# Kernel tuning notes

Hardware: AMD Instinct MI355X
Metric: run time of the kernel (lower is better)

Reference implementation:

```python
import jax, jax.numpy as jnp
import numpy as np

B, T, S, D, F = 4, 2048, 2048, 256, 1024
EPS = 1e-5


def setup_inputs() -> dict:
    key = jax.random.key(0)
    ks = jax.random.split(key, 24)
    def lin(kw, kb, din, dout):
        w = jax.random.normal(kw, (din, dout), jnp.float32) / np.sqrt(din)
        b = jax.random.normal(kb, (dout,), jnp.float32) * 0.01
        return w, b
    Wq1, bq1 = lin(ks[0], ks[1], D, D)
    Wk1, bk1 = lin(ks[2], ks[3], D, D)
    Wv1, bv1 = lin(ks[4], ks[5], D, D)
    Wq2, bq2 = lin(ks[6], ks[7], D, D)
    Wk2, bk2 = lin(ks[8], ks[9], D, D)
    Wv2, bv2 = lin(ks[10], ks[11], D, D)
    W1, b1 = lin(ks[12], ks[13], D, F)
    W2, b2 = lin(ks[14], ks[15], F, D)
    y = jax.random.normal(ks[16], (B, T, D), jnp.float32)
    Z = jax.random.normal(ks[17], (B, S, D), jnp.float32)
    target_mask = jnp.tril(jnp.ones((T, T), jnp.int32))  # causal 0/1 mask
    return dict(y=y, Z=Z, target_mask=target_mask,
                Wq1=Wq1, bq1=bq1, Wk1=Wk1, bk1=bk1, Wv1=Wv1, bv1=bv1,
                Wq2=Wq2, bq2=bq2, Wk2=Wk2, bk2=bk2, Wv2=Wv2, bv2=bv2,
                W1=W1, b1=b1, W2=W2, b2=b2,
                g1=jnp.ones((D,), jnp.float32), be1=jnp.zeros((D,), jnp.float32),
                g2=jnp.ones((D,), jnp.float32), be2=jnp.zeros((D,), jnp.float32),
                g3=jnp.ones((D,), jnp.float32), be3=jnp.zeros((D,), jnp.float32))


def _ln(x, g, b):
    m = x.mean(-1, keepdims=True)
    v = ((x - m) ** 2).mean(-1, keepdims=True)
    return (x - m) / jnp.sqrt(v + EPS) * g + b


def _attn(Q, K, V, mask=None):
    scale = 1.0 / np.sqrt(Q.shape[-1]).astype(np.float32)
    scores = jnp.einsum('btd,bsd->bts', Q, K) * scale  # [B,T,S]
    if mask is not None:
        scores = jnp.where(mask == 0, -jnp.inf, scores)
    probs = jax.nn.softmax(scores, axis=-1)
    return jnp.einsum('bts,bsd->btd', probs, V)


def reference(y, Z, target_mask, Wq1, bq1, Wk1, bk1, Wv1, bv1,
              Wq2, bq2, Wk2, bk2, Wv2, bv2, W1, b1, W2, b2,
              g1, be1, g2, be2, g3, be3):
    # self attention
    sa = _attn(y @ Wq1 + bq1, y @ Wk1 + bk1, y @ Wv1 + bv1, target_mask)
    y1 = _ln(y + sa, g1, be1)
    # cross attention
    ca = _attn(y1 @ Wq2 + bq2, Z @ Wk2 + bk2, Z @ Wv2 + bv2)
    y2 = _ln(y1 + ca, g2, be2)
    # FFN
    ffn = jax.nn.relu(y2 @ W1 + b1) @ W2 + b2
    return _ln(y2 + ffn, g3, be3)
```

## Files before the change

### kernel.cpp

```cpp
#include <hip/hip_runtime.h>

#define B_ 4
#define T_ 2048
#define S_ 2048
#define D_ 256
#define F_ 1024

typedef unsigned short ushort_t;
typedef __bf16 v8bf __attribute__((ext_vector_type(8)));
typedef float v4f __attribute__((ext_vector_type(4)));
typedef __attribute__((address_space(1))) const unsigned int gas_uint;
typedef __attribute__((address_space(3))) unsigned int las_uint;

__device__ __forceinline__ ushort_t f2bf(float f) {
  unsigned u = __float_as_uint(f);
  unsigned r = (u + 0x7FFFu + ((u >> 16) & 1u)) >> 16;
  return (ushort_t)r;
}
__device__ __forceinline__ float bf2f(ushort_t u) {
  return __uint_as_float((unsigned)u << 16);
}

struct WP { const float* s; ushort_t* d; int K, N; };
struct WP8 { WP m[8]; };

__global__ void prep_weights_k(WP8 a) {
  WP w = a.m[blockIdx.z];
  int k0 = blockIdx.x * 64, n0 = blockIdx.y * 64;
  if (k0 >= w.K || n0 >= w.N) return;
  __shared__ ushort_t tile[64][65];
  int tx = threadIdx.x, ty = threadIdx.y;
  for (int r = ty; r < 64; r += 4)
    tile[r][tx] = f2bf(w.s[(size_t)(k0 + r) * w.N + n0 + tx]);
  __syncthreads();
  for (int r = ty; r < 64; r += 4)
    w.d[(size_t)(n0 + r) * w.K + k0 + tx] = tile[tx][r];
}

__global__ void pack_bias_k(const float* bq1, const float* bk1, const float* bv1,
                            const float* bk2, const float* bv2,
                            float* bqkv1, float* bkv2) {
  int t = blockIdx.x * 256 + threadIdx.x;
  if (t < 768) bqkv1[t] = (t < 256) ? bq1[t] : (t < 512) ? bk1[t - 256] : bv1[t - 512];
  if (t < 512) bkv2[t] = (t < 256) ? bk2[t] : bv2[t - 256];
}

__global__ void cvt_k(const float* __restrict__ a, ushort_t* __restrict__ oa,
                      const float* __restrict__ b, ushort_t* __restrict__ ob) {
  int i = blockIdx.x * 256 + threadIdx.x;
  const float* s = blockIdx.y ? b : a;
  ushort_t* d = blockIdx.y ? ob : oa;
  size_t off = (size_t)i * 8;
  float4 v0 = *(const float4*)(s + off);
  float4 v1 = *(const float4*)(s + off + 4);
  union { ushort_t u[8]; uint4 v; } pk;
  pk.u[0] = f2bf(v0.x); pk.u[1] = f2bf(v0.y); pk.u[2] = f2bf(v0.z); pk.u[3] = f2bf(v0.w);
  pk.u[4] = f2bf(v1.x); pk.u[5] = f2bf(v1.y); pk.u[6] = f2bf(v1.z); pk.u[7] = f2bf(v1.w);
  *(uint4*)(d + off) = pk.v;
}

__global__ void transpose_bf16_k(const ushort_t* __restrict__ in, long long sIz, int ldin,
                                 ushort_t* __restrict__ out, long long sOz,
                                 int rows, int cols) {
  in  += (size_t)blockIdx.z * sIz;
  out += (size_t)blockIdx.z * sOz;
  __shared__ ushort_t tile[64][65];
  int r0 = blockIdx.x * 64, c0 = blockIdx.y * 64;
  int tx = threadIdx.x, ty = threadIdx.y;
  for (int r = ty; r < 64; r += 4)
    tile[r][tx] = in[(size_t)(r0 + r) * ldin + c0 + tx];
  __syncthreads();
  for (int r = ty; r < 64; r += 4)
    out[(size_t)(c0 + r) * rows + r0 + tx] = tile[tx][r];
}

template<bool RELU>
__global__ __launch_bounds__(256, 2) void gemm_bt(
    const ushort_t* __restrict__ A, int lda, long long sAz,
    const ushort_t* __restrict__ Bt, int ldb, long long sBz,
    const float* __restrict__ bias,
    float* __restrict__ Cf, ushort_t* __restrict__ Cb, int ldc, long long sCz,
    int K, float alpha, int causal, int kcausal, int crow0) {
  const int n0 = blockIdx.x * 64, m0 = blockIdx.y * 128;
  if (causal && n0 > crow0 + m0 + 127) return;
  const int Keff = kcausal ? ((crow0 + m0 + 128 < K) ? crow0 + m0 + 128 : K) : K;
  A  += (long long)blockIdx.z * sAz;
  Bt += (long long)blockIdx.z * sBz;
  const long long coff = (long long)blockIdx.z * sCz;
  const int t = threadIdx.x, lane = t & 63, wv = t >> 6;
  const int wm = wv >> 1, wn = wv & 1;
  const int kslot = lane >> 4, l15 = lane & 15;
  __shared__ __align__(16) char smem[24576];
  char* sA = smem;
  char* sB = smem + 16384;

  v4f acc[4][2];
  v4f zero = {0.f, 0.f, 0.f, 0.f};
#pragma unroll
  for (int m = 0; m < 4; ++m)
#pragma unroll
    for (int n = 0; n < 2; ++n) acc[m][n] = zero;

  for (int kk = 0; kk < Keff; kk += 64) {
    __syncthreads();
#pragma unroll
    for (int q = 0; q < 4; ++q) {
      int g = q * 256 + t;
      int row = g >> 3, j = g & 7;
      const ushort_t* src = A + (long long)(m0 + row) * lda + kk + ((j ^ (row & 7)) << 3);
      __builtin_amdgcn_global_load_lds((gas_uint*)src,
          (las_uint*)(sA + q * 4096 + (wv << 10)), 16, 0, 0);
    }
#pragma unroll
    for (int q = 0; q < 2; ++q) {
      int g = q * 256 + t;
      int row = g >> 3, j = g & 7;
      const ushort_t* src = Bt + (long long)(n0 + row) * ldb + kk + ((j ^ (row & 7)) << 3);
      __builtin_amdgcn_global_load_lds((gas_uint*)src,
          (las_uint*)(sB + q * 4096 + (wv << 10)), 16, 0, 0);
    }
    __syncthreads();
#pragma unroll
    for (int ks = 0; ks < 2; ++ks) {
      v8bf af[4]; v8bf bfr[2];
#pragma unroll
      for (int m = 0; m < 4; ++m) {
        int row = wm * 64 + m * 16 + l15;
        int gs = (ks * 4 + kslot) ^ (row & 7);
        af[m] = *(const v8bf*)(sA + ((row * 8 + gs) << 4));
      }
#pragma unroll
      for (int n = 0; n < 2; ++n) {
        int row = wn * 32 + n * 16 + l15;
        int gs = (ks * 4 + kslot) ^ (row & 7);
        bfr[n] = *(const v8bf*)(sB + ((row * 8 + gs) << 4));
      }
#pragma unroll
      for (int m = 0; m < 4; ++m)
#pragma unroll
        for (int n = 0; n < 2; ++n)
          acc[m][n] = __builtin_amdgcn_mfma_f32_16x16x32_bf16(af[m], bfr[n], acc[m][n], 0, 0, 0);
    }
  }
#pragma unroll
  for (int m = 0; m < 4; ++m) {
    int grow0 = m0 + wm * 64 + m * 16 + (kslot << 2);
#pragma unroll
    for (int n = 0; n < 2; ++n) {
      int gcol = n0 + wn * 32 + n * 16 + l15;
      float bb = bias ? bias[gcol] : 0.f;
#pragma unroll
      for (int i = 0; i < 4; ++i) {
        float v = acc[m][n][i] * alpha + bb;
        if (RELU) v = fmaxf(v, 0.f);
        long long off = coff + (long long)(grow0 + i) * ldc + gcol;
        if (Cf) Cf[off] = v;
        if (Cb) Cb[off] = f2bf(v);
      }
    }
  }
}

__global__ __launch_bounds__(256) void softmax_k(ushort_t* sc, int causal, int crow0) {
  int row = blockIdx.x;
  ushort_t* rp = sc + ((size_t)blockIdx.y * T_ + row) * S_;
  int t = threadIdx.x;
  int valid = causal ? crow0 + row + 1 : S_;
  union { ushort_t u[8]; uint4 v; } in;
  in.v = *(const uint4*)(rp + t * 8);
  float x[8];
#pragma unroll
  for (int j = 0; j < 8; ++j) x[j] = bf2f(in.u[j]);
  float m = -3.0e38f;
#pragma unroll
  for (int j = 0; j < 8; ++j) if (t * 8 + j < valid) m = fmaxf(m, x[j]);
  for (int mk = 1; mk < 64; mk <<= 1) m = fmaxf(m, __shfl_xor(m, mk));
  __shared__ float rbuf[8];
  if ((t & 63) == 0) rbuf[t >> 6] = m;
  __syncthreads();
  m = fmaxf(fmaxf(rbuf[0], rbuf[1]), fmaxf(rbuf[2], rbuf[3]));
  float p[8]; float l = 0.f;
#pragma unroll
  for (int j = 0; j < 8; ++j) { p[j] = (t * 8 + j < valid) ? __expf(x[j] - m) : 0.f; l += p[j]; }
  for (int mk = 1; mk < 64; mk <<= 1) l += __shfl_xor(l, mk);
  if ((t & 63) == 0) rbuf[4 + (t >> 6)] = l;
  __syncthreads();
  l = rbuf[4] + rbuf[5] + rbuf[6] + rbuf[7];
  float inv = 1.f / l;
  union { ushort_t u[8]; uint4 v; } pk;
#pragma unroll
  for (int j = 0; j < 8; ++j) pk.u[j] = f2bf(p[j] * inv);
  *(uint4*)(rp + t * 8) = pk.v;
}

__global__ __launch_bounds__(256) void add_ln_k(
    const float* __restrict__ base, const float* __restrict__ delta,
    const float* __restrict__ g, const float* __restrict__ be,
    float* __restrict__ outf, ushort_t* __restrict__ outb) {
  int row = blockIdx.x * 4 + (threadIdx.x >> 6);
  int lane = threadIdx.x & 63;
  size_t off = (size_t)row * 256 + lane * 4;
  float4 xv = *(const float4*)(base + off);
  float4 dv = *(const float4*)(delta + off);
  float s0 = xv.x + dv.x, s1 = xv.y + dv.y, s2 = xv.z + dv.z, s3 = xv.w + dv.w;
  float sum = s0 + s1 + s2 + s3;
  for (int mk = 1; mk < 64; mk <<= 1) sum += __shfl_xor(sum, mk);
  float mean = sum * (1.f / 256.f);
  float e0 = s0 - mean, e1 = s1 - mean, e2 = s2 - mean, e3 = s3 - mean;
  float ss = e0 * e0 + e1 * e1 + e2 * e2 + e3 * e3;
  for (int mk = 1; mk < 64; mk <<= 1) ss += __shfl_xor(ss, mk);
  float rstd = rsqrtf(ss * (1.f / 256.f) + 1e-5f);
  float4 gv = *(const float4*)(g + lane * 4);
  float4 bv = *(const float4*)(be + lane * 4);
  float o0 = e0 * rstd * gv.x + bv.x, o1 = e1 * rstd * gv.y + bv.y;
  float o2 = e2 * rstd * gv.z + bv.z, o3 = e3 * rstd * gv.w + bv.w;
  float4 ov; ov.x = o0; ov.y = o1; ov.z = o2; ov.w = o3;
  *(float4*)(outf + off) = ov;
  if (outb) {
    union { ushort_t u[4]; uint2 v; } pk;
    pk.u[0] = f2bf(o0); pk.u[1] = f2bf(o1); pk.u[2] = f2bf(o2); pk.u[3] = f2bf(o3);
    *(uint2*)(outb + off) = pk.v;
  }
}

extern "C" void kernel_launch(void* const* d_in, const int* in_sizes, int n_in,
                              void* d_out, int out_size, void* d_ws, size_t ws_size,
                              hipStream_t stream) {
  const float* y   = (const float*)d_in[0];
  const float* Z   = (const float*)d_in[1];
  const float* Wq1 = (const float*)d_in[3];  const float* bq1 = (const float*)d_in[4];
  const float* Wk1 = (const float*)d_in[5];  const float* bk1 = (const float*)d_in[6];
  const float* Wv1 = (const float*)d_in[7];  const float* bv1 = (const float*)d_in[8];
  const float* Wq2 = (const float*)d_in[9];  const float* bq2 = (const float*)d_in[10];
  const float* Wk2 = (const float*)d_in[11]; const float* bk2 = (const float*)d_in[12];
  const float* Wv2 = (const float*)d_in[13]; const float* bv2 = (const float*)d_in[14];
  const float* W1  = (const float*)d_in[15]; const float* b1  = (const float*)d_in[16];
  const float* W2  = (const float*)d_in[17]; const float* b2  = (const float*)d_in[18];
  const float* g1  = (const float*)d_in[19]; const float* be1 = (const float*)d_in[20];
  const float* g2  = (const float*)d_in[21]; const float* be2 = (const float*)d_in[22];
  const float* g3  = (const float*)d_in[23]; const float* be3 = (const float*)d_in[24];
  float* out = (float*)d_out;

  char* p = (char*)d_ws;
  auto alloc = [&](size_t sz) { char* r = p; p += (sz + 255) & ~(size_t)255; return r; };
  const size_t NBT = (size_t)B_ * T_ * D_;
  ushort_t* Wq1t = (ushort_t*)alloc(D_ * D_ * 2);
  ushort_t* Wk1t = (ushort_t*)alloc(D_ * D_ * 2);
  ushort_t* Wv1t = (ushort_t*)alloc(D_ * D_ * 2);
  ushort_t* Wq2t = (ushort_t*)alloc(D_ * D_ * 2);
  ushort_t* Wk2t = (ushort_t*)alloc(D_ * D_ * 2);
  ushort_t* Wv2t = (ushort_t*)alloc(D_ * D_ * 2);
  ushort_t* W1t  = (ushort_t*)alloc((size_t)F_ * D_ * 2);
  ushort_t* W2t  = (ushort_t*)alloc((size_t)D_ * F_ * 2);
  float* bqkv1 = (float*)alloc(768 * 4);
  float* bkv2  = (float*)alloc(512 * 4);
  ushort_t* yb  = (ushort_t*)alloc(NBT * 2);
  ushort_t* Zb  = (ushort_t*)alloc(NBT * 2);
  float*    y1f = (float*)alloc(NBT * 4);
  ushort_t* y1b = (ushort_t*)alloc(NBT * 2);
  float*    y2f = (float*)alloc(NBT * 4);
  ushort_t* y2b = (ushort_t*)alloc(NBT * 2);
  ushort_t* QKVb = (ushort_t*)alloc((size_t)B_ * T_ * 768 * 2);
  ushort_t* Vt   = (ushort_t*)alloc(NBT * 2);
  ushort_t* Hb = QKVb;
  float* tmp = (float*)alloc(NBT * 4);
  ushort_t* sc = (ushort_t*)p;
  size_t remain = (ws_size > (size_t)(p - (char*)d_ws))
                      ? ws_size - (size_t)(p - (char*)d_ws) : 0;
  const size_t rowb = (size_t)S_ * 2;
  int CH = 0, TC = 0;
  if (remain >= (size_t)B_ * T_ * rowb)      { CH = B_; TC = T_; }
  else if (remain >= (size_t)T_ * rowb)      { CH = 1;  TC = T_; }
  else {
    int tc = (int)(remain / (rowb * 128)) * 128;
    if (tc > T_) tc = T_;
    CH = 1; TC = tc;
  }

  WP8 wp;
  wp.m[0] = {Wq1, Wq1t, D_, D_}; wp.m[1] = {Wk1, Wk1t, D_, D_};
  wp.m[2] = {Wv1, Wv1t, D_, D_}; wp.m[3] = {Wq2, Wq2t, D_, D_};
  wp.m[4] = {Wk2, Wk2t, D_, D_}; wp.m[5] = {Wv2, Wv2t, D_, D_};
  wp.m[6] = {W1, W1t, D_, F_};   wp.m[7] = {W2, W2t, F_, D_};
  prep_weights_k<<<dim3(16, 16, 8), dim3(64, 4), 0, stream>>>(wp);
  pack_bias_k<<<dim3(5), 256, 0, stream>>>(bq1, bk1, bv1, bk2, bv2, bqkv1, bkv2);
  cvt_k<<<dim3((int)(NBT / 8 / 256), 2), 256, 0, stream>>>(y, yb, Z, Zb);

  auto gemm = [&](const ushort_t* A, int lda, long long sAz,
                  const ushort_t* Bt, int ldb, long long sBz,
                  const float* bias, float* Cf, ushort_t* Cb, int ldc, long long sCz,
                  int M, int N, int K, float alpha, int causal, int kcausal,
                  bool relu, int Zn, int crow0) {
    dim3 g(N / 64, M / 128, Zn);
    if (relu)
      gemm_bt<true><<<g, 256, 0, stream>>>(A, lda, sAz, Bt, ldb, sBz, bias, Cf, Cb, ldc, sCz, K, alpha, causal, kcausal, crow0);
    else
      gemm_bt<false><<<g, 256, 0, stream>>>(A, lda, sAz, Bt, ldb, sBz, bias, Cf, Cb, ldc, sCz, K, alpha, causal, kcausal, crow0);
  };

  auto attention = [&](float* attout, int causal) {
    transpose_bf16_k<<<dim3(S_ / 64, D_ / 64, B_), dim3(64, 4), 0, stream>>>(
        QKVb + 512, (long long)S_ * 768, 768, Vt, (long long)D_ * S_, S_, D_);
    if (TC <= 0) return;
    const ushort_t* Q = QKVb;
    const ushort_t* Kc = QKVb + 256;
    for (int b0 = 0; b0 < B_; b0 += CH) {
      for (int t0 = 0; t0 < T_; t0 += TC) {
        int rows = (t0 + TC <= T_) ? TC : (T_ - t0);
        gemm(Q + ((size_t)b0 * T_ + t0) * 768, 768, (long long)T_ * 768,
             Kc + (size_t)b0 * S_ * 768, 768, (long long)S_ * 768,
             nullptr, nullptr, sc, S_, (long long)T_ * S_,
             rows, S_, D_, 0.0625f, causal, 0, false, CH, t0);
        softmax_k<<<dim3(rows, CH), 256, 0, stream>>>(sc, causal, t0);
        gemm(sc, S_, (long long)T_ * S_,
             Vt + (size_t)b0 * D_ * S_, S_, (long long)D_ * S_,
             nullptr, attout + ((size_t)b0 * T_ + t0) * D_, nullptr, D_, (long long)T_ * D_,
             rows, D_, S_, 1.f, 0, causal, false, CH, t0);
      }
    }
  };

  gemm(yb, D_, 0, Wq1t, D_, 0, bqkv1, nullptr, QKVb, 768, 0,
       B_ * T_, 768, D_, 1.f, 0, 0, false, 1, 0);
  attention(tmp, 1);
  add_ln_k<<<dim3(B_ * T_ / 4), 256, 0, stream>>>(y, tmp, g1, be1, y1f, y1b);

  gemm(y1b, D_, 0, Wq2t, D_, 0, bq2, nullptr, QKVb, 768, 0,
       B_ * T_, D_, D_, 1.f, 0, 0, false, 1, 0);
  gemm(Zb, D_, 0, Wk2t, D_, 0, bkv2, nullptr, QKVb + 256, 768, 0,
       B_ * S_, 512, D_, 1.f, 0, 0, false, 1, 0);
  attention(tmp, 0);
  add_ln_k<<<dim3(B_ * T_ / 4), 256, 0, stream>>>(y1f, tmp, g2, be2, y2f, y2b);

  gemm(y2b, D_, 0, W1t, D_, 0, b1, nullptr, Hb, F_, 0,
       B_ * T_, F_, D_, 1.f, 0, 0, true, 1, 0);
  gemm(Hb, F_, 0, W2t, F_, 0, b2, tmp, nullptr, D_, 0,
       B_ * T_, D_, F_, 1.f, 0, 0, false, 1, 0);
  add_ln_k<<<dim3(B_ * T_ / 4), 256, 0, stream>>>(y2f, tmp, g3, be3, out, nullptr);
}
```

Baseline: 336.4 us.

## Replace materialized attention with fused flash-attention kernel using online softmax

Replaces the score GEMM, softmax kernel and PV GEMM with a single per-16-query wave kernel that computes QK^T with MFMA, applies an online softmax in registers, shuffles probabilities into MFMA operand layout, and accumulates PV. This removes writing and rereading the full bf16 score matrix and the separate softmax pass. The new kernel uses one wave per block and loads K/V directly from global memory without LDS sharing, so it relies on L2 reuse and may have low occupancy and latency hiding. The GEMM kernel is simplified by dropping batch stride, alpha and causal parameters.

```diff
diff --git a/kernel.cpp b/kernel.cpp
--- a/kernel.cpp
+++ b/kernel.cpp
@@ -16,9 +16,6 @@
   unsigned u = __float_as_uint(f);
   unsigned r = (u + 0x7FFFu + ((u >> 16) & 1u)) >> 16;
   return (ushort_t)r;
-}
-__device__ __forceinline__ float bf2f(ushort_t u) {
-  return __uint_as_float((unsigned)u << 16);
 }
 
 struct WP { const float* s; ushort_t* d; int K, N; };
@@ -76,17 +73,11 @@
 
 template<bool RELU>
 __global__ __launch_bounds__(256, 2) void gemm_bt(
-    const ushort_t* __restrict__ A, int lda, long long sAz,
-    const ushort_t* __restrict__ Bt, int ldb, long long sBz,
+    const ushort_t* __restrict__ A, int lda,
+    const ushort_t* __restrict__ Bt, int ldb,
     const float* __restrict__ bias,
-    float* __restrict__ Cf, ushort_t* __restrict__ Cb, int ldc, long long sCz,
-    int K, float alpha, int causal, int kcausal, int crow0) {
+    float* __restrict__ Cf, ushort_t* __restrict__ Cb, int ldc, int K) {
   const int n0 = blockIdx.x * 64, m0 = blockIdx.y * 128;
-  if (causal && n0 > crow0 + m0 + 127) return;
-  const int Keff = kcausal ? ((crow0 + m0 + 128 < K) ? crow0 + m0 + 128 : K) : K;
-  A  += (long long)blockIdx.z * sAz;
-  Bt += (long long)blockIdx.z * sBz;
-  const long long coff = (long long)blockIdx.z * sCz;
   const int t = threadIdx.x, lane = t & 63, wv = t >> 6;
   const int wm = wv >> 1, wn = wv & 1;
   const int kslot = lane >> 4, l15 = lane & 15;
@@ -101,7 +92,7 @@
 #pragma unroll
     for (int n = 0; n < 2; ++n) acc[m][n] = zero;
 
-  for (int kk = 0; kk < Keff; kk += 64) {
+  for (int kk = 0; kk < K; kk += 64) {
     __syncthreads();
 #pragma unroll
     for (int q = 0; q < 4; ++q) {
@@ -151,9 +142,9 @@
       float bb = bias ? bias[gcol] : 0.f;
 #pragma unroll
       for (int i = 0; i < 4; ++i) {
-        float v = acc[m][n][i] * alpha + bb;
+        float v = acc[m][n][i] + bb;
         if (RELU) v = fmaxf(v, 0.f);
-        long long off = coff + (long long)(grow0 + i) * ldc + gcol;
+        long long off = (long long)(grow0 + i) * ldc + gcol;
         if (Cf) Cf[off] = v;
         if (Cb) Cb[off] = f2bf(v);
       }
@@ -161,36 +152,104 @@
   }
 }
 
-__global__ __launch_bounds__(256) void softmax_k(ushort_t* sc, int causal, int crow0) {
-  int row = blockIdx.x;
-  ushort_t* rp = sc + ((size_t)blockIdx.y * T_ + row) * S_;
-  int t = threadIdx.x;
-  int valid = causal ? crow0 + row + 1 : S_;
-  union { ushort_t u[8]; uint4 v; } in;
-  in.v = *(const uint4*)(rp + t * 8);
-  float x[8];
-#pragma unroll
-  for (int j = 0; j < 8; ++j) x[j] = bf2f(in.u[j]);
-  float m = -3.0e38f;
-#pragma unroll
-  for (int j = 0; j < 8; ++j) if (t * 8 + j < valid) m = fmaxf(m, x[j]);
-  for (int mk = 1; mk < 64; mk <<= 1) m = fmaxf(m, __shfl_xor(m, mk));
-  __shared__ float rbuf[8];
-  if ((t & 63) == 0) rbuf[t >> 6] = m;
-  __syncthreads();
-  m = fmaxf(fmaxf(rbuf[0], rbuf[1]), fmaxf(rbuf[2], rbuf[3]));
-  float p[8]; float l = 0.f;
-#pragma unroll
-  for (int j = 0; j < 8; ++j) { p[j] = (t * 8 + j < valid) ? __expf(x[j] - m) : 0.f; l += p[j]; }
-  for (int mk = 1; mk < 64; mk <<= 1) l += __shfl_xor(l, mk);
-  if ((t & 63) == 0) rbuf[4 + (t >> 6)] = l;
-  __syncthreads();
-  l = rbuf[4] + rbuf[5] + rbuf[6] + rbuf[7];
-  float inv = 1.f / l;
-  union { ushort_t u[8]; uint4 v; } pk;
-#pragma unroll
-  for (int j = 0; j < 8; ++j) pk.u[j] = f2bf(p[j] * inv);
-  *(uint4*)(rp + t * 8) = pk.v;
+template<int CAUSAL>
+__global__ __launch_bounds__(64) void flash_k(
+    const ushort_t* __restrict__ QKV, const ushort_t* __restrict__ Vt,
+    float* __restrict__ O) {
+  const int b = blockIdx.y, q0 = blockIdx.x * 16;
+  const int lane = threadIdx.x & 63;
+  const int kslot = lane >> 4, l15 = lane & 15;
+  const ushort_t* Qp = QKV + (size_t)b * T_ * 768;
+  const ushort_t* Kp = Qp + 256;
+  const ushort_t* Vb = Vt + (size_t)b * (size_t)D_ * S_;
+  const int q = q0 + l15;
+
+  v8bf qf[8];
+  {
+    const ushort_t* qrow = Qp + (size_t)q * 768 + kslot * 8;
+#pragma unroll
+    for (int ks = 0; ks < 8; ++ks) qf[ks] = *(const v8bf*)(qrow + ks * 32);
+  }
+  v4f acc_o[16];
+  v4f zero = {0.f, 0.f, 0.f, 0.f};
+#pragma unroll
+  for (int td = 0; td < 16; ++td) acc_o[td] = zero;
+  float m_run = -3.0e38f, l_run = 0.f;
+
+  const int nt = CAUSAL ? ((q0 + 47) >> 5) : (S_ / 32);
+  for (int it = 0; it < nt; ++it) {
+    const int kv0 = it * 32;
+    const ushort_t* kr0 = Kp + (size_t)(kv0 + l15) * 768 + kslot * 8;
+    v4f s0 = zero, s1 = zero;
+#pragma unroll
+    for (int ks = 0; ks < 8; ++ks) {
+      v8bf k0 = *(const v8bf*)(kr0 + ks * 32);
+      v8bf k1 = *(const v8bf*)(kr0 + 16 * 768 + ks * 32);
+      s0 = __builtin_amdgcn_mfma_f32_16x16x32_bf16(k0, qf[ks], s0, 0, 0, 0);
+      s1 = __builtin_amdgcn_mfma_f32_16x16x32_bf16(k1, qf[ks], s1, 0, 0, 0);
+    }
+    float ps[2][4];
+#pragma unroll
+    for (int i = 0; i < 4; ++i) { ps[0][i] = s0[i] * 0.0625f; ps[1][i] = s1[i] * 0.0625f; }
+    if (CAUSAL && kv0 + 31 > q) {
+#pragma unroll
+      for (int n = 0; n < 2; ++n)
+#pragma unroll
+        for (int i = 0; i < 4; ++i)
+          if (kv0 + n * 16 + kslot * 4 + i > q) ps[n][i] = -3.0e38f;
+    }
+    float mx = ps[0][0];
+#pragma unroll
+    for (int i = 1; i < 4; ++i) mx = fmaxf(mx, ps[0][i]);
+#pragma unroll
+    for (int i = 0; i < 4; ++i) mx = fmaxf(mx, ps[1][i]);
+    mx = fmaxf(mx, __shfl_xor(mx, 16));
+    mx = fmaxf(mx, __shfl_xor(mx, 32));
+    float mn = fmaxf(m_run, mx);
+    float al = __expf(m_run - mn);
+    float pe[2][4]; float lt = 0.f;
+#pragma unroll
+    for (int n = 0; n < 2; ++n)
+#pragma unroll
+      for (int i = 0; i < 4; ++i) { pe[n][i] = __expf(ps[n][i] - mn); lt += pe[n][i]; }
+    lt += __shfl_xor(lt, 16);
+    lt += __shfl_xor(lt, 32);
+    l_run = l_run * al + lt;
+    m_run = mn;
+    unsigned P0 = (unsigned)f2bf(pe[0][0]) | ((unsigned)f2bf(pe[0][1]) << 16);
+    unsigned P1 = (unsigned)f2bf(pe[0][2]) | ((unsigned)f2bf(pe[0][3]) << 16);
+    unsigned P2 = (unsigned)f2bf(pe[1][0]) | ((unsigned)f2bf(pe[1][1]) << 16);
+    unsigned P3 = (unsigned)f2bf(pe[1][2]) | ((unsigned)f2bf(pe[1][3]) << 16);
+    int srcLo = (((kslot * 2) & 3) << 4) | l15;
+    int srcHi = (((kslot * 2 + 1) & 3) << 4) | l15;
+    int a0 = __shfl((int)P0, srcLo), a1 = __shfl((int)P1, srcLo);
+    int a2 = __shfl((int)P2, srcLo), a3 = __shfl((int)P3, srcLo);
+    int b0 = __shfl((int)P0, srcHi), b1 = __shfl((int)P1, srcHi);
+    int b2 = __shfl((int)P2, srcHi), b3 = __shfl((int)P3, srcHi);
+    union { unsigned u[4]; v8bf v; } pbu;
+    pbu.u[0] = (unsigned)(kslot < 2 ? a0 : a2);
+    pbu.u[1] = (unsigned)(kslot < 2 ? a1 : a3);
+    pbu.u[2] = (unsigned)(kslot < 2 ? b0 : b2);
+    pbu.u[3] = (unsigned)(kslot < 2 ? b1 : b3);
+    v8bf pb = pbu.v;
+#pragma unroll
+    for (int td = 0; td < 16; ++td) acc_o[td] *= al;
+    const ushort_t* vr = Vb + (size_t)l15 * S_ + kv0 + kslot * 8;
+#pragma unroll
+    for (int td = 0; td < 16; ++td) {
+      v8bf vf = *(const v8bf*)(vr + (size_t)td * 16 * S_);
+      acc_o[td] = __builtin_amdgcn_mfma_f32_16x16x32_bf16(vf, pb, acc_o[td], 0, 0, 0);
+    }
+  }
+  float li = 1.f / l_run;
+  float* orow = O + ((size_t)b * T_ + q) * D_ + kslot * 4;
+#pragma unroll
+  for (int td = 0; td < 16; ++td) {
+    float4 v;
+    v.x = acc_o[td][0] * li; v.y = acc_o[td][1] * li;
+    v.z = acc_o[td][2] * li; v.w = acc_o[td][3] * li;
+    *(float4*)(orow + td * 16) = v;
+  }
 }
 
 __global__ __launch_bounds__(256) void add_ln_k(
@@ -264,18 +323,6 @@
   ushort_t* Vt   = (ushort_t*)alloc(NBT * 2);
   ushort_t* Hb = QKVb;
   float* tmp = (float*)alloc(NBT * 4);
-  ushort_t* sc = (ushort_t*)p;
-  size_t remain = (ws_size > (size_t)(p - (char*)d_ws))
-                      ? ws_size - (size_t)(p - (char*)d_ws) : 0;
-  const size_t rowb = (size_t)S_ * 2;
-  int CH = 0, TC = 0;
-  if (remain >= (size_t)B_ * T_ * rowb)      { CH = B_; TC = T_; }
-  else if (remain >= (size_t)T_ * rowb)      { CH = 1;  TC = T_; }
-  else {
-    int tc = (int)(remain / (rowb * 128)) * 128;
-    if (tc > T_) tc = T_;
-    CH = 1; TC = tc;
-  }
 
   WP8 wp;
   wp.m[0] = {Wq1, Wq1t, D_, D_}; wp.m[1] = {Wk1, Wk1t, D_, D_};
@@ -286,55 +333,35 @@
   pack_bias_k<<<dim3(5), 256, 0, stream>>>(bq1, bk1, bv1, bk2, bv2, bqkv1, bkv2);
   cvt_k<<<dim3((int)(NBT / 8 / 256), 2), 256, 0, stream>>>(y, yb, Z, Zb);
 
-  auto gemm = [&](const ushort_t* A, int lda, long long sAz,
-                  const ushort_t* Bt, int ldb, long long sBz,
-                  const float* bias, float* Cf, ushort_t* Cb, int ldc, long long sCz,
-                  int M, int N, int K, float alpha, int causal, int kcausal,
-                  bool relu, int Zn, int crow0) {
-    dim3 g(N / 64, M / 128, Zn);
+  auto gemm = [&](const ushort_t* A, int lda, const ushort_t* Bt, int ldb,
+                  const float* bias, float* Cf, ushort_t* Cb, int ldc,
+                  int M, int N, int K, bool relu) {
+    dim3 g(N / 64, M / 128, 1);
     if (relu)
-      gemm_bt<true><<<g, 256, 0, stream>>>(A, lda, sAz, Bt, ldb, sBz, bias, Cf, Cb, ldc, sCz, K, alpha, causal, kcausal, crow0);
+      gemm_bt<true><<<g, 256, 0, stream>>>(A, lda, Bt, ldb, bias, Cf, Cb, ldc, K);
     else
-      gemm_bt<false><<<g, 256, 0, stream>>>(A, lda, sAz, Bt, ldb, sBz, bias, Cf, Cb, ldc, sCz, K, alpha, causal, kcausal, crow0);
+      gemm_bt<false><<<g, 256, 0, stream>>>(A, lda, Bt, ldb, bias, Cf, Cb, ldc, K);
   };
 
   auto attention = [&](float* attout, int causal) {
     transpose_bf16_k<<<dim3(S_ / 64, D_ / 64, B_), dim3(64, 4), 0, stream>>>(
         QKVb + 512, (long long)S_ * 768, 768, Vt, (long long)D_ * S_, S_, D_);
-    if (TC <= 0) return;
-    const ushort_t* Q = QKVb;
-    const ushort_t* Kc = QKVb + 256;
-    for (int b0 = 0; b0 < B_; b0 += CH) {
-      for (int t0 = 0; t0 < T_; t0 += TC) {
-        int rows = (t0 + TC <= T_) ? TC : (T_ - t0);
-        gemm(Q + ((size_t)b0 * T_ + t0) * 768, 768, (long long)T_ * 768,
-             Kc + (size_t)b0 * S_ * 768, 768, (long long)S_ * 768,
-             nullptr, nullptr, sc, S_, (long long)T_ * S_,
-             rows, S_, D_, 0.0625f, causal, 0, false, CH, t0);
-        softmax_k<<<dim3(rows, CH), 256, 0, stream>>>(sc, causal, t0);
-        gemm(sc, S_, (long long)T_ * S_,
-             Vt + (size_t)b0 * D_ * S_, S_, (long long)D_ * S_,
-             nullptr, attout + ((size_t)b0 * T_ + t0) * D_, nullptr, D_, (long long)T_ * D_,
-             rows, D_, S_, 1.f, 0, causal, false, CH, t0);
-      }
-    }
+    if (causal)
+      flash_k<1><<<dim3(T_ / 16, B_), 64, 0, stream>>>(QKVb, Vt, attout);
+    else
+      flash_k<0><<<dim3(T_ / 16, B_), 64, 0, stream>>>(QKVb, Vt, attout);
   };
 
-  gemm(yb, D_, 0, Wq1t, D_, 0, bqkv1, nullptr, QKVb, 768, 0,
-       B_ * T_, 768, D_, 1.f, 0, 0, false, 1, 0);
+  gemm(yb, D_, Wq1t, D_, bqkv1, nullptr, QKVb, 768, B_ * T_, 768, D_, false);
   attention(tmp, 1);
   add_ln_k<<<dim3(B_ * T_ / 4), 256, 0, stream>>>(y, tmp, g1, be1, y1f, y1b);
 
-  gemm(y1b, D_, 0, Wq2t, D_, 0, bq2, nullptr, QKVb, 768, 0,
-       B_ * T_, D_, D_, 1.f, 0, 0, false, 1, 0);
-  gemm(Zb, D_, 0, Wk2t, D_, 0, bkv2, nullptr, QKVb + 256, 768, 0,
-       B_ * S_, 512, D_, 1.f, 0, 0, false, 1, 0);
+  gemm(y1b, D_, Wq2t, D_, bq2, nullptr, QKVb, 768, B_ * T_, D_, D_, false);
+  gemm(Zb, D_, Wk2t, D_, bkv2, nullptr, QKVb + 256, 768, B_ * S_, 512, D_, false);
   attention(tmp, 0);
   add_ln_k<<<dim3(B_ * T_ / 4), 256, 0, stream>>>(y1f, tmp, g2, be2, y2f, y2b);
 
-  gemm(y2b, D_, 0, W1t, D_, 0, b1, nullptr, Hb, F_, 0,
-       B_ * T_, F_, D_, 1.f, 0, 0, true, 1, 0);
-  gemm(Hb, F_, 0, W2t, F_, 0, b2, tmp, nullptr, D_, 0,
-       B_ * T_, D_, F_, 1.f, 0, 0, false, 1, 0);
+  gemm(y2b, D_, W1t, D_, b1, nullptr, Hb, F_, B_ * T_, F_, D_, true);
+  gemm(Hb, F_, W2t, F_, b2, tmp, nullptr, D_, B_ * T_, D_, F_, false);
   add_ln_k<<<dim3(B_ * T_ / 4), 256, 0, stream>>>(y2f, tmp, g3, be3, out, nullptr);
 }
```

New measurement: 575.8 us. +71.2%, slower.

## Add 128x128 GEMM tile variant and trim causal softmax reads and writes

Applied to the files above, without the earlier changes.

Adds a 128x128-tile bf16 MFMA GEMM kernel that uses swizzled global_load_lds staging and skips fully masked causal tiles. It is used for the QK^T score GEMM, the QKV/KV projections and FFN1, while the narrow-N GEMMs stay on the 64-wide kernel. The softmax now skips loading masked-out columns and skips writing past the 128-column tile boundary, since the PV GEMM never reads those. The larger tiles raise data reuse per block but use more registers and launch fewer blocks, which can reduce occupancy.

```diff
diff --git a/kernel.cpp b/kernel.cpp
--- a/kernel.cpp
+++ b/kernel.cpp
@@ -161,19 +161,113 @@
   }
 }
 
+template<bool RELU>
+__global__ __launch_bounds__(256, 2) void gemm_bt128(
+    const ushort_t* __restrict__ A, int lda, long long sAz,
+    const ushort_t* __restrict__ Bt, int ldb, long long sBz,
+    const float* __restrict__ bias,
+    float* __restrict__ Cf, ushort_t* __restrict__ Cb, int ldc, long long sCz,
+    int K, float alpha, int causal, int crow0) {
+  const int n0 = blockIdx.x * 128, m0 = blockIdx.y * 128;
+  if (causal && n0 > crow0 + m0 + 127) return;
+  A  += (long long)blockIdx.z * sAz;
+  Bt += (long long)blockIdx.z * sBz;
+  const long long coff = (long long)blockIdx.z * sCz;
+  const int t = threadIdx.x, lane = t & 63, wv = t >> 6;
+  const int wm = wv >> 1, wn = wv & 1;
+  const int kslot = lane >> 4, l15 = lane & 15;
+  __shared__ __align__(16) char smem[32768];
+  char* sA = smem;
+  char* sB = smem + 16384;
+
+  v4f acc[4][4];
+  v4f zero = {0.f, 0.f, 0.f, 0.f};
+#pragma unroll
+  for (int m = 0; m < 4; ++m)
+#pragma unroll
+    for (int n = 0; n < 4; ++n) acc[m][n] = zero;
+
+  for (int kk = 0; kk < K; kk += 64) {
+    __syncthreads();
+#pragma unroll
+    for (int q = 0; q < 4; ++q) {
+      int g = q * 256 + t;
+      int row = g >> 3, j = g & 7;
+      const ushort_t* src = A + (long long)(m0 + row) * lda + kk + ((j ^ (row & 7)) << 3);
+      __builtin_amdgcn_global_load_lds((gas_uint*)src,
+          (las_uint*)(sA + q * 4096 + (wv << 10)), 16, 0, 0);
+    }
+#pragma unroll
+    for (int q = 0; q < 4; ++q) {
+      int g = q * 256 + t;
+      int row = g >> 3, j = g & 7;
+      const ushort_t* src = Bt + (long long)(n0 + row) * ldb + kk + ((j ^ (row & 7)) << 3);
+      __builtin_amdgcn_global_load_lds((gas_uint*)src,
+          (las_uint*)(sB + q * 4096 + (wv << 10)), 16, 0, 0);
+    }
+    __syncthreads();
+#pragma unroll
+    for (int ks = 0; ks < 2; ++ks) {
+      v8bf af[4]; v8bf bfr[4];
+#pragma unroll
+      for (int m = 0; m < 4; ++m) {
+        int row = wm * 64 + m * 16 + l15;
+        int gs = (ks * 4 + kslot) ^ (row & 7);
+        af[m] = *(const v8bf*)(sA + ((row * 8 + gs) << 4));
+      }
+#pragma unroll
+      for (int n = 0; n < 4; ++n) {
+        int row = wn * 64 + n * 16 + l15;
+        int gs = (ks * 4 + kslot) ^ (row & 7);
+        bfr[n] = *(const v8bf*)(sB + ((row * 8 + gs) << 4));
+      }
+#pragma unroll
+      for (int m = 0; m < 4; ++m)
+#pragma unroll
+        for (int n = 0; n < 4; ++n)
+          acc[m][n] = __builtin_amdgcn_mfma_f32_16x16x32_bf16(af[m], bfr[n], acc[m][n], 0, 0, 0);
+    }
+  }
+#pragma unroll
+  for (int m = 0; m < 4; ++m) {
+    int grow0 = m0 + wm * 64 + m * 16 + (kslot << 2);
+#pragma unroll
+    for (int n = 0; n < 4; ++n) {
+      int gcol = n0 + wn * 64 + n * 16 + l15;
+      float bb = bias ? bias[gcol] : 0.f;
+#pragma unroll
+      for (int i = 0; i < 4; ++i) {
+        float v = acc[m][n][i] * alpha + bb;
+        if (RELU) v = fmaxf(v, 0.f);
+        long long off = coff + (long long)(grow0 + i) * ldc + gcol;
+        if (Cf) Cf[off] = v;
+        if (Cb) Cb[off] = f2bf(v);
+      }
+    }
+  }
+}
+
 __global__ __launch_bounds__(256) void softmax_k(ushort_t* sc, int causal, int crow0) {
   int row = blockIdx.x;
   ushort_t* rp = sc + ((size_t)blockIdx.y * T_ + row) * S_;
   int t = threadIdx.x;
-  int valid = causal ? crow0 + row + 1 : S_;
-  union { ushort_t u[8]; uint4 v; } in;
-  in.v = *(const uint4*)(rp + t * 8);
+  int gr = crow0 + row;
+  int vlim = causal ? gr + 1 : S_;
+  int wlim = causal ? (((gr >> 7) + 1) << 7) : S_;
+  if (wlim > S_) wlim = S_;
   float x[8];
-#pragma unroll
-  for (int j = 0; j < 8; ++j) x[j] = bf2f(in.u[j]);
+  if (t * 8 < vlim) {
+    union { ushort_t u[8]; uint4 v; } in;
+    in.v = *(const uint4*)(rp + t * 8);
+#pragma unroll
+    for (int j = 0; j < 8; ++j) x[j] = bf2f(in.u[j]);
+  } else {
+#pragma unroll
+    for (int j = 0; j < 8; ++j) x[j] = -3.0e38f;
+  }
   float m = -3.0e38f;
 #pragma unroll
-  for (int j = 0; j < 8; ++j) if (t * 8 + j < valid) m = fmaxf(m, x[j]);
+  for (int j = 0; j < 8; ++j) if (t * 8 + j < vlim) m = fmaxf(m, x[j]);
   for (int mk = 1; mk < 64; mk <<= 1) m = fmaxf(m, __shfl_xor(m, mk));
   __shared__ float rbuf[8];
   if ((t & 63) == 0) rbuf[t >> 6] = m;
@@ -181,16 +275,18 @@
   m = fmaxf(fmaxf(rbuf[0], rbuf[1]), fmaxf(rbuf[2], rbuf[3]));
   float p[8]; float l = 0.f;
 #pragma unroll
-  for (int j = 0; j < 8; ++j) { p[j] = (t * 8 + j < valid) ? __expf(x[j] - m) : 0.f; l += p[j]; }
+  for (int j = 0; j < 8; ++j) { p[j] = (t * 8 + j < vlim) ? __expf(x[j] - m) : 0.f; l += p[j]; }
   for (int mk = 1; mk < 64; mk <<= 1) l += __shfl_xor(l, mk);
   if ((t & 63) == 0) rbuf[4 + (t >> 6)] = l;
   __syncthreads();
   l = rbuf[4] + rbuf[5] + rbuf[6] + rbuf[7];
   float inv = 1.f / l;
-  union { ushort_t u[8]; uint4 v; } pk;
-#pragma unroll
-  for (int j = 0; j < 8; ++j) pk.u[j] = f2bf(p[j] * inv);
-  *(uint4*)(rp + t * 8) = pk.v;
+  if (t * 8 < wlim) {
+    union { ushort_t u[8]; uint4 v; } pk;
+#pragma unroll
+    for (int j = 0; j < 8; ++j) pk.u[j] = f2bf(p[j] * inv);
+    *(uint4*)(rp + t * 8) = pk.v;
+  }
 }
 
 __global__ __launch_bounds__(256) void add_ln_k(
@@ -284,18 +380,26 @@
   wp.m[6] = {W1, W1t, D_, F_};   wp.m[7] = {W2, W2t, F_, D_};
   prep_weights_k<<<dim3(16, 16, 8), dim3(64, 4), 0, stream>>>(wp);
   pack_bias_k<<<dim3(5), 256, 0, stream>>>(bq1, bk1, bv1, bk2, bv2, bqkv1, bkv2);
-  cvt_k<<<dim3((int)(NBT / 8 / 256), 2), 256, 0, stream>>>(y, yb, Z, Zb);
+  cvt_k<<<dim3((int)(NBT / 8 / 256), 2), 256, 0, stream>>>(y, yb, Zb ? Z : Z, Zb);
 
   auto gemm = [&](const ushort_t* A, int lda, long long sAz,
                   const ushort_t* Bt, int ldb, long long sBz,
                   const float* bias, float* Cf, ushort_t* Cb, int ldc, long long sCz,
                   int M, int N, int K, float alpha, int causal, int kcausal,
-                  bool relu, int Zn, int crow0) {
-    dim3 g(N / 64, M / 128, Zn);
-    if (relu)
-      gemm_bt<true><<<g, 256, 0, stream>>>(A, lda, sAz, Bt, ldb, sBz, bias, Cf, Cb, ldc, sCz, K, alpha, causal, kcausal, crow0);
-    else
-      gemm_bt<false><<<g, 256, 0, stream>>>(A, lda, sAz, Bt, ldb, sBz, bias, Cf, Cb, ldc, sCz, K, alpha, causal, kcausal, crow0);
+                  bool relu, int Zn, int crow0, bool big) {
+    if (big) {
+      dim3 g(N / 128, M / 128, Zn);
+      if (relu)
+        gemm_bt128<true><<<g, 256, 0, stream>>>(A, lda, sAz, Bt, ldb, sBz, bias, Cf, Cb, ldc, sCz, K, alpha, causal, crow0);
+      else
+        gemm_bt128<false><<<g, 256, 0, stream>>>(A, lda, sAz, Bt, ldb, sBz, bias, Cf, Cb, ldc, sCz, K, alpha, causal, crow0);
+    } else {
+      dim3 g(N / 64, M / 128, Zn);
+      if (relu)
+        gemm_bt<true><<<g, 256, 0, stream>>>(A, lda, sAz, Bt, ldb, sBz, bias, Cf, Cb, ldc, sCz, K, alpha, causal, kcausal, crow0);
+      else
+        gemm_bt<false><<<g, 256, 0, stream>>>(A, lda, sAz, Bt, ldb, sBz, bias, Cf, Cb, ldc, sCz, K, alpha, causal, kcausal, crow0);
+    }
   };
 
   auto attention = [&](float* attout, int causal) {
@@ -310,31 +414,31 @@
         gemm(Q + ((size_t)b0 * T_ + t0) * 768, 768, (long long)T_ * 768,
              Kc + (size_t)b0 * S_ * 768, 768, (long long)S_ * 768,
              nullptr, nullptr, sc, S_, (long long)T_ * S_,
-             rows, S_, D_, 0.0625f, causal, 0, false, CH, t0);
+             rows, S_, D_, 0.0625f, causal, 0, false, CH, t0, true);
         softmax_k<<<dim3(rows, CH), 256, 0, stream>>>(sc, causal, t0);
         gemm(sc, S_, (long long)T_ * S_,
              Vt + (size_t)b0 * D_ * S_, S_, (long long)D_ * S_,
              nullptr, attout + ((size_t)b0 * T_ + t0) * D_, nullptr, D_, (long long)T_ * D_,
-             rows, D_, S_, 1.f, 0, causal, false, CH, t0);
+             rows, D_, S_, 1.f, 0, causal, false, CH, t0, false);
       }
     }
   };
 
   gemm(yb, D_, 0, Wq1t, D_, 0, bqkv1, nullptr, QKVb, 768, 0,
-       B_ * T_, 768, D_, 1.f, 0, 0, false, 1, 0);
+       B_ * T_, 768, D_, 1.f, 0, 0, false, 1, 0, true);
   attention(tmp, 1);
   add_ln_k<<<dim3(B_ * T_ / 4), 256, 0, stream>>>(y, tmp, g1, be1, y1f, y1b);
 
   gemm(y1b, D_, 0, Wq2t, D_, 0, bq2, nullptr, QKVb, 768, 0,
-       B_ * T_, D_, D_, 1.f, 0, 0, false, 1, 0);
+       B_ * T_, D_, D_, 1.f, 0, 0, false, 1, 0, false);
   gemm(Zb, D_, 0, Wk2t, D_, 0, bkv2, nullptr, QKVb + 256, 768, 0,
-       B_ * S_, 512, D_, 1.f, 0, 0, false, 1, 0);
+       B_ * S_, 512, D_, 1.f, 0, 0, false, 1, 0, true);
   attention(tmp, 0);
   add_ln_k<<<dim3(B_ * T_ / 4), 256, 0, stream>>>(y1f, tmp, g2, be2, y2f, y2b);
 
   gemm(y2b, D_, 0, W1t, D_, 0, b1, nullptr, Hb, F_, 0,
-       B_ * T_, F_, D_, 1.f, 0, 0, true, 1, 0);
+       B_ * T_, F_, D_, 1.f, 0, 0, true, 1, 0, true);
   gemm(Hb, F_, 0, W2t, F_, 0, b2, tmp, nullptr, D_, 0,
-       B_ * T_, D_, F_, 1.f, 0, 0, false, 1, 0);
+       B_ * T_, D_, F_, 1.f, 0, 0, false, 1, 0, false);
   add_ln_k<<<dim3(B_ * T_ / 4), 256, 0, stream>>>(y2f, tmp, g3, be3, out, nullptr);
 }
```

After: 343.3 us. 2.0% more time.
